# Kernel tuning notes

Measured on AMD Instinct MI355X. Metric: run time of the kernel, lower is better.

Reference implementation:

```python
import jax, jax.numpy as jnp
import numpy as np

NUM_REGIONS = 32   # region labels are 1..NUM_REGIONS, 0 = background
EPS = 1e-8


def setup_inputs() -> dict:
    key = jax.random.key(0)
    k1, k2 = jax.random.split(key)
    B, D, H, W = 4, 160, 192, 192
    x = jax.random.normal(k1, (B, 1, D, H, W), dtype=jnp.float32)
    # precomputed connected-component label map (0 = background)
    region_map = jax.random.randint(k2, (B, D, H, W), 0, NUM_REGIONS + 1, dtype=jnp.int32)
    return {"x": x, "region_map": region_map}


def _per_volume_sums(xf, seg):
    # xf: [V] sigmoid probs, seg: [V] region ids in [0, NUM_REGIONS]
    xs = jax.ops.segment_sum(xf, seg, num_segments=NUM_REGIONS + 1)
    cnt = jax.ops.segment_sum(jnp.ones_like(xf), seg, num_segments=NUM_REGIONS + 1)
    return xs, cnt


def reference(x, region_map):
    B = x.shape[0]
    probs = jax.nn.sigmoid(x)                      # x.dim()==5 -> sigmoid
    xf = probs.reshape(B, -1)                      # [B, V]
    seg = region_map.reshape(B, -1)                # [B, V]
    xs, cnt = jax.vmap(_per_volume_sums)(xf, seg)  # [B, R+1] each
    xs_r = xs[:, 1:]                               # per-region sum of sigmoid(x)
    cnt_r = cnt[:, 1:]                             # per-region voxel count (= sum of binary y)
    # dice over the region: y==1 inside the region, so intersection == xs_r
    dice = 2.0 * xs_r / (xs_r + cnt_r + EPS)       # [B, R]
    valid = cnt_r > 0                              # region actually present
    n_valid = jnp.sum(valid, axis=-1)              # [B]
    mean_dice = jnp.sum(jnp.where(valid, dice, 0.0), axis=-1) / jnp.maximum(n_valid, 1)
    loss_b = jnp.where(n_valid > 0, 1.0 - mean_dice, 1.0)  # num_features==0 -> loss 1.0
    return jnp.mean(loss_b)
```

## Files before the change

### kernel.cpp

```cpp
#include <hip/hip_runtime.h>

#define NUM_REGIONS 32
#define NBINS 33
#define BATCH 4
#define DHW (160*192*192)
#define NVEC_PER_BATCH (DHW/4)
#define BLOCKS_PER_BATCH 256
#define NBLOCKS (BATCH*BLOCKS_PER_BATCH)
#define VEC_PER_BLOCK (NVEC_PER_BATCH/BLOCKS_PER_BATCH)
#define ITERS 23
#define HCOLS 256
#define RED_STRIDE 257
#define QSCALE 262144.0f
#define INV_QSCALE (1.0f/262144.0f)
#define CNT_SHIFT 25
#define XS_MASK ((1u<<CNT_SHIFT)-1u)
#define EPS 1e-8f

__global__ __launch_bounds__(256) void region_sums_kernel(
    const float* __restrict__ x,
    const int*   __restrict__ seg,
    float*       __restrict__ ws)
{
    __shared__ unsigned int hist[NBINS * HCOLS];
    __shared__ float part_xs [8][32];
    __shared__ float part_cnt[8][32];

    float acc[32];
    #pragma unroll
    for (int b = 0; b < 32; ++b) acc[b] = 0.0f;

    const int tid = threadIdx.x;

    for (int i = tid; i < NBINS * HCOLS; i += 256) hist[i] = 0u;
    __syncthreads();

    const int batch = blockIdx.x >> 8;
    const int local = blockIdx.x & 255;
    const int vbase = batch * NVEC_PER_BATCH + local * VEC_PER_BLOCK;

    const float4* __restrict__ xv4 = (const float4*)x;
    const int4*   __restrict__ sv4 = (const int4*)seg;

    #define OFFK(k) ((((k)*256 + tid) < VEC_PER_BLOCK) ? ((k)*256 + tid) : (VEC_PER_BLOCK-1))

    float4 xA = xv4[vbase + OFFK(0)]; int4 sA = sv4[vbase + OFFK(0)];
    float4 xB = xv4[vbase + OFFK(1)]; int4 sB = sv4[vbase + OFFK(1)];

    #pragma unroll 1
    for (int k = 0; k < ITERS; ++k) {
        const int kn = (k + 2 < ITERS) ? (k + 2) : (ITERS - 1);
        float4 xN = xv4[vbase + OFFK(kn)];
        int4   sN = sv4[vbase + OFFK(kn)];

        float e0 = __expf(-xA.x);
        float e1 = __expf(-xA.y);
        float e2 = __expf(-xA.z);
        float e3 = __expf(-xA.w);
        float p0 = __builtin_amdgcn_rcpf(1.0f + e0);
        float p1 = __builtin_amdgcn_rcpf(1.0f + e1);
        float p2 = __builtin_amdgcn_rcpf(1.0f + e2);
        float p3 = __builtin_amdgcn_rcpf(1.0f + e3);

        const bool active = (k * 256 + tid) < VEC_PER_BLOCK;
        if (active) {
            unsigned qz = (unsigned)(fmaf(p2, QSCALE, 0.5f)) + (1u << CNT_SHIFT);
            unsigned qw = (unsigned)(fmaf(p3, QSCALE, 0.5f)) + (1u << CNT_SHIFT);
            atomicAdd(&hist[sA.z * HCOLS + tid], qz);
            atomicAdd(&hist[sA.w * HCOLS + tid], qw);

            float P0 = p0 + 256.0f;
            float P1 = p1 + 256.0f;
            #pragma unroll
            for (int b = 0; b < 32; ++b) {
                acc[b] += (sA.x == b + 1) ? P0 : 0.0f;
                acc[b] += (sA.y == b + 1) ? P1 : 0.0f;
            }
        }

        xA = xB; sA = sB; xB = xN; sB = sN;
    }
    #undef OFFK
    __syncthreads();

    float h_xs, h_cnt;
    {
        const int bin = (tid & 31) + 1;
        const int g   = tid >> 5;
        float xs = 0.0f, cnt = 0.0f;
        #pragma unroll
        for (int j = 0; j < 32; ++j) {
            const int col = g * 32 + ((j + bin) & 31);
            unsigned V = hist[bin * HCOLS + col];
            cnt += (float)(V >> CNT_SHIFT);
            xs  += (float)(V & XS_MASK);
        }
        h_xs  = xs * INV_QSCALE;
        h_cnt = cnt;
    }
    __syncthreads();

    float* redf = (float*)hist;

    #pragma unroll
    for (int b = 0; b < 32; ++b) redf[b * RED_STRIDE + tid] = acc[b];
    __syncthreads();
    {
        const int bin = tid & 31;
        const int g   = tid >> 5;
        float xs = 0.0f, cnt = 0.0f;
        #pragma unroll
        for (int j = 0; j < 32; ++j) {
            float V = redf[bin * RED_STRIDE + g * 32 + j];
            float c = truncf(V * (1.0f / 256.0f));
            cnt += c;
            xs  += V - 256.0f * c;
        }
        part_xs [g][bin] = xs;
        part_cnt[g][bin] = cnt;
    }
    __syncthreads();

    if (tid < 32) {
        float xs = 0.0f, cnt = 0.0f;
        #pragma unroll
        for (int g = 0; g < 8; ++g) {
            xs  += part_xs [g][tid];
            cnt += part_cnt[g][tid];
        }
        atomicAdd(&ws[batch * NBINS + tid + 1], xs);
        atomicAdd(&ws[BATCH * NBINS + batch * NBINS + tid + 1], cnt);
    }
    __syncthreads();

    {
        const int bin = tid & 31;
        const int g   = tid >> 5;
        part_xs [g][bin] = h_xs;
        part_cnt[g][bin] = h_cnt;
    }
    __syncthreads();
    if (tid < 32) {
        float xs = 0.0f, cnt = 0.0f;
        #pragma unroll
        for (int g = 0; g < 8; ++g) {
            xs  += part_xs [g][tid];
            cnt += part_cnt[g][tid];
        }
        atomicAdd(&ws[batch * NBINS + tid + 1], xs);
        atomicAdd(&ws[BATCH * NBINS + batch * NBINS + tid + 1], cnt);
    }
}

__global__ void region_dice_final_kernel(
    const float* __restrict__ ws,
    float*       __restrict__ out)
{
    const int lane = threadIdx.x;
    float loss_sum = 0.0f;

    for (int b = 0; b < BATCH; ++b) {
        bool  valid = false;
        float dice  = 0.0f;
        if (lane >= 1 && lane <= NUM_REGIONS) {
            float xs  = ws[b * NBINS + lane];
            float cnt = ws[BATCH * NBINS + b * NBINS + lane];
            valid = (cnt > 0.0f);
            if (valid) dice = 2.0f * xs / (xs + cnt + EPS);
        }
        unsigned long long m = __ballot(valid);
        int n_valid = __popcll(m);

        float s = dice;
        #pragma unroll
        for (int off = 32; off >= 1; off >>= 1) s += __shfl_down(s, off);

        float mean_dice = s / (float)((n_valid > 1) ? n_valid : 1);
        float loss_b    = (n_valid > 0) ? (1.0f - mean_dice) : 1.0f;
        loss_sum += loss_b;
    }

    if (lane == 0) out[0] = loss_sum * (1.0f / BATCH);
}

extern "C" void kernel_launch(void* const* d_in, const int* in_sizes, int n_in,
                              void* d_out, int out_size, void* d_ws, size_t ws_size,
                              hipStream_t stream)
{
    const float* x   = (const float*)d_in[0];
    const int*   seg = (const int*)d_in[1];
    float*       ws  = (float*)d_ws;

    hipMemsetAsync(d_ws, 0, 2 * BATCH * NBINS * sizeof(float), stream);

    region_sums_kernel<<<NBLOCKS, 256, 0, stream>>>(x, seg, ws);
    region_dice_final_kernel<<<1, 64, 0, stream>>>(ws, (float*)d_out);
}
```

Before: 222.0 us.

## Specialize waves into VALU-accumulate and LDS-atomic groups with uneven work split

```diff
diff --git a/kernel.cpp b/kernel.cpp
--- a/kernel.cpp
+++ b/kernel.cpp
@@ -8,9 +8,12 @@
 #define BLOCKS_PER_BATCH 256
 #define NBLOCKS (BATCH*BLOCKS_PER_BATCH)
 #define VEC_PER_BLOCK (NVEC_PER_BATCH/BLOCKS_PER_BATCH)
-#define ITERS 23
-#define HCOLS 256
-#define RED_STRIDE 257
+#define VALU_VECS 3200
+#define ITERS_V 25
+#define DS_VECS 2560
+#define ITERS_D 20
+#define HCOLS 128
+#define RED_STRIDE 129
 #define QSCALE 262144.0f
 #define INV_QSCALE (1.0f/262144.0f)
 #define CNT_SHIFT 25
@@ -26,92 +29,116 @@
     __shared__ float part_xs [8][32];
     __shared__ float part_cnt[8][32];
 
+    const int tid = threadIdx.x;
+
+    for (int i = tid; i < NBINS * HCOLS; i += 256) hist[i] = 0u;
+    __syncthreads();
+
+    const int batch = blockIdx.x >> 8;
+    const int local = blockIdx.x & 255;
+    const int vbase = batch * NVEC_PER_BATCH + local * VEC_PER_BLOCK;
+
+    const float4* __restrict__ xv4 = (const float4*)x;
+    const int4*   __restrict__ sv4 = (const int4*)seg;
+
     float acc[32];
     #pragma unroll
     for (int b = 0; b < 32; ++b) acc[b] = 0.0f;
 
-    const int tid = threadIdx.x;
-
-    for (int i = tid; i < NBINS * HCOLS; i += 256) hist[i] = 0u;
-    __syncthreads();
-
-    const int batch = blockIdx.x >> 8;
-    const int local = blockIdx.x & 255;
-    const int vbase = batch * NVEC_PER_BATCH + local * VEC_PER_BLOCK;
-
-    const float4* __restrict__ xv4 = (const float4*)x;
-    const int4*   __restrict__ sv4 = (const int4*)seg;
-
-    #define OFFK(k) ((((k)*256 + tid) < VEC_PER_BLOCK) ? ((k)*256 + tid) : (VEC_PER_BLOCK-1))
-
-    float4 xA = xv4[vbase + OFFK(0)]; int4 sA = sv4[vbase + OFFK(0)];
-    float4 xB = xv4[vbase + OFFK(1)]; int4 sB = sv4[vbase + OFFK(1)];
-
-    #pragma unroll 1
-    for (int k = 0; k < ITERS; ++k) {
-        const int kn = (k + 2 < ITERS) ? (k + 2) : (ITERS - 1);
-        float4 xN = xv4[vbase + OFFK(kn)];
-        int4   sN = sv4[vbase + OFFK(kn)];
-
-        float e0 = __expf(-xA.x);
-        float e1 = __expf(-xA.y);
-        float e2 = __expf(-xA.z);
-        float e3 = __expf(-xA.w);
-        float p0 = __builtin_amdgcn_rcpf(1.0f + e0);
-        float p1 = __builtin_amdgcn_rcpf(1.0f + e1);
-        float p2 = __builtin_amdgcn_rcpf(1.0f + e2);
-        float p3 = __builtin_amdgcn_rcpf(1.0f + e3);
-
-        const bool active = (k * 256 + tid) < VEC_PER_BLOCK;
-        if (active) {
-            unsigned qz = (unsigned)(fmaf(p2, QSCALE, 0.5f)) + (1u << CNT_SHIFT);
-            unsigned qw = (unsigned)(fmaf(p3, QSCALE, 0.5f)) + (1u << CNT_SHIFT);
-            atomicAdd(&hist[sA.z * HCOLS + tid], qz);
-            atomicAdd(&hist[sA.w * HCOLS + tid], qw);
-
-            float P0 = p0 + 256.0f;
-            float P1 = p1 + 256.0f;
+    if (tid < 128) {
+        const int base = vbase + tid;
+        float4 xA = xv4[base];       int4 sA = sv4[base];
+        float4 xB = xv4[base + 128]; int4 sB = sv4[base + 128];
+
+        #pragma unroll 1
+        for (int k = 0; k < ITERS_V; ++k) {
+            const int kn = (k + 2 < ITERS_V) ? (k + 2) : (ITERS_V - 1);
+            float4 xN = xv4[base + kn * 128];
+            int4   sN = sv4[base + kn * 128];
+
+            float P0 = __builtin_amdgcn_rcpf(1.0f + __expf(-xA.x)) + 256.0f;
+            float P1 = __builtin_amdgcn_rcpf(1.0f + __expf(-xA.y)) + 256.0f;
+            float P2 = __builtin_amdgcn_rcpf(1.0f + __expf(-xA.z)) + 256.0f;
+            float P3 = __builtin_amdgcn_rcpf(1.0f + __expf(-xA.w)) + 256.0f;
+
             #pragma unroll
             for (int b = 0; b < 32; ++b) {
                 acc[b] += (sA.x == b + 1) ? P0 : 0.0f;
                 acc[b] += (sA.y == b + 1) ? P1 : 0.0f;
+                acc[b] += (sA.z == b + 1) ? P2 : 0.0f;
+                acc[b] += (sA.w == b + 1) ? P3 : 0.0f;
             }
-        }
-
-        xA = xB; sA = sB; xB = xN; sB = sN;
-    }
-    #undef OFFK
-    __syncthreads();
-
-    float h_xs, h_cnt;
+
+            xA = xB; sA = sB; xB = xN; sB = sN;
+        }
+    } else {
+        const int lane2 = tid - 128;
+        const int base  = vbase + VALU_VECS + lane2;
+        float4 xA = xv4[base];       int4 sA = sv4[base];
+        float4 xB = xv4[base + 128]; int4 sB = sv4[base + 128];
+
+        #pragma unroll 1
+        for (int k = 0; k < ITERS_D; ++k) {
+            const int kn = (k + 2 < ITERS_D) ? (k + 2) : (ITERS_D - 1);
+            float4 xN = xv4[base + kn * 128];
+            int4   sN = sv4[base + kn * 128];
+
+            float p0 = __builtin_amdgcn_rcpf(1.0f + __expf(-xA.x));
+            float p1 = __builtin_amdgcn_rcpf(1.0f + __expf(-xA.y));
+            float p2 = __builtin_amdgcn_rcpf(1.0f + __expf(-xA.z));
+            float p3 = __builtin_amdgcn_rcpf(1.0f + __expf(-xA.w));
+
+            unsigned q0 = (unsigned)(fmaf(p0, QSCALE, 0.5f)) + (1u << CNT_SHIFT);
+            unsigned q1 = (unsigned)(fmaf(p1, QSCALE, 0.5f)) + (1u << CNT_SHIFT);
+            unsigned q2 = (unsigned)(fmaf(p2, QSCALE, 0.5f)) + (1u << CNT_SHIFT);
+            unsigned q3 = (unsigned)(fmaf(p3, QSCALE, 0.5f)) + (1u << CNT_SHIFT);
+
+            atomicAdd(&hist[sA.x * HCOLS + lane2], q0);
+            atomicAdd(&hist[sA.y * HCOLS + lane2], q1);
+            atomicAdd(&hist[sA.z * HCOLS + lane2], q2);
+            atomicAdd(&hist[sA.w * HCOLS + lane2], q3);
+
+            xA = xB; sA = sB; xB = xN; sB = sN;
+        }
+    }
+    __syncthreads();
+
     {
         const int bin = (tid & 31) + 1;
         const int g   = tid >> 5;
         float xs = 0.0f, cnt = 0.0f;
         #pragma unroll
-        for (int j = 0; j < 32; ++j) {
-            const int col = g * 32 + ((j + bin) & 31);
+        for (int j = 0; j < 16; ++j) {
+            const int col = g * 16 + ((j + bin) & 15);
             unsigned V = hist[bin * HCOLS + col];
             cnt += (float)(V >> CNT_SHIFT);
             xs  += (float)(V & XS_MASK);
         }
-        h_xs  = xs * INV_QSCALE;
-        h_cnt = cnt;
-    }
-    __syncthreads();
-
+        part_xs [g][bin - 1] = xs * INV_QSCALE;
+        part_cnt[g][bin - 1] = cnt;
+    }
+    __syncthreads();
+
+    float hxs = 0.0f, hcnt = 0.0f;
+    if (tid < 32) {
+        #pragma unroll
+        for (int g = 0; g < 8; ++g) { hxs += part_xs[g][tid]; hcnt += part_cnt[g][tid]; }
+    }
     float* redf = (float*)hist;
-
-    #pragma unroll
-    for (int b = 0; b < 32; ++b) redf[b * RED_STRIDE + tid] = acc[b];
-    __syncthreads();
+    if (tid < 128) {
+        #pragma unroll
+        for (int b = 0; b < 32; ++b) redf[b * RED_STRIDE + tid] = acc[b];
+    }
+    __syncthreads();
+
     {
         const int bin = tid & 31;
         const int g   = tid >> 5;
         float xs = 0.0f, cnt = 0.0f;
         #pragma unroll
-        for (int j = 0; j < 32; ++j) {
-            float V = redf[bin * RED_STRIDE + g * 32 + j];
+        for (int j = 0; j < 16; ++j) {
+            const int col = g * 16 + ((j + bin) & 15);
+            float V = redf[bin * RED_STRIDE + col];
             float c = truncf(V * (1.0f / 256.0f));
             cnt += c;
             xs  += V - 256.0f * c;
@@ -122,31 +149,9 @@
     __syncthreads();
 
     if (tid < 32) {
-        float xs = 0.0f, cnt = 0.0f;
-        #pragma unroll
-        for (int g = 0; g < 8; ++g) {
-            xs  += part_xs [g][tid];
-            cnt += part_cnt[g][tid];
-        }
-        atomicAdd(&ws[batch * NBINS + tid + 1], xs);
-        atomicAdd(&ws[BATCH * NBINS + batch * NBINS + tid + 1], cnt);
-    }
-    __syncthreads();
-
-    {
-        const int bin = tid & 31;
-        const int g   = tid >> 5;
-        part_xs [g][bin] = h_xs;
-        part_cnt[g][bin] = h_cnt;
-    }
-    __syncthreads();
-    if (tid < 32) {
-        float xs = 0.0f, cnt = 0.0f;
-        #pragma unroll
-        for (int g = 0; g < 8; ++g) {
-            xs  += part_xs [g][tid];
-            cnt += part_cnt[g][tid];
-        }
+        float xs = hxs, cnt = hcnt;
+        #pragma unroll
+        for (int g = 0; g < 8; ++g) { xs += part_xs[g][tid]; cnt += part_cnt[g][tid]; }
         atomicAdd(&ws[batch * NBINS + tid + 1], xs);
         atomicAdd(&ws[BATCH * NBINS + batch * NBINS + tid + 1], cnt);
     }
```

Measured after the change: 220.8 us. No clear change (-0.5%).
